# Kernel tuning notes

Measured on AMD Instinct MI355X. Metric: run time of the kernel, lower is better.

## Reference

```python
import jax, jax.numpy as jnp
import numpy as np

WEIGHT = 1.0
BIN_SIZE = 1.0
MAX_MZ = 2000.0
NUM_BINS = int(MAX_MZ / BIN_SIZE)  # 2000
B, N = 8192, 256


def setup_inputs() -> dict:
    key = jax.random.key(0)
    k1, k2, k3, k4, k5 = jax.random.split(key, 5)
    return {
        "pred_mz": jax.random.uniform(k1, (B, N), dtype=jnp.float32),
        "pred_intensity": jax.random.uniform(k2, (B, N), dtype=jnp.float32),
        "target_mz": jax.random.uniform(k3, (B, N), dtype=jnp.float32),
        "target_intensity": jax.random.uniform(k4, (B, N), dtype=jnp.float32),
        "target_mask": jax.random.uniform(k5, (B, N), dtype=jnp.float32),
    }


def _bin_spectrum(mz, intensity):
    # mz is normalized to [0,1]; denormalize and bin. Batched scatter-add:
    # a single 2D indexed add replaces the per-sample scatter_add_ loop.
    bin_idx = jnp.clip((mz * MAX_MZ / BIN_SIZE).astype(jnp.int32), 0, NUM_BINS - 1)  # [B, N]
    bsz = mz.shape[0]
    binned = jnp.zeros((bsz, NUM_BINS), dtype=intensity.dtype)
    return binned.at[jnp.arange(bsz)[:, None], bin_idx].add(intensity)


def reference(pred_mz, pred_intensity, target_mz, target_intensity, target_mask):
    pred_binned = _bin_spectrum(pred_mz, pred_intensity)                    # [B, NUM_BINS]
    target_binned = _bin_spectrum(target_mz, target_intensity * target_mask)
    eps = 1e-8  # matches torch F.cosine_similarity default
    pn = jnp.maximum(jnp.linalg.norm(pred_binned, axis=1), eps)
    tn = jnp.maximum(jnp.linalg.norm(target_binned, axis=1), eps)
    cos = jnp.sum(pred_binned * target_binned, axis=1) / (pn * tn)
    cos = jnp.clip(cos, -1.0, 1.0)
    angle = jnp.arccos(cos)
    loss = jnp.mean(angle / jnp.pi)
    return WEIGHT * loss
```

## Files before the change

kernel.cpp:

```cpp
#include <hip/hip_runtime.h>
#include <math.h>


#define SAL_NUM_BINS 2000
#define SAL_B 8192
#define SAL_N 256
#define SAL_RPB 2
#define SAL_BLOCKS (SAL_B / SAL_RPB)

__global__ __launch_bounds__(256) void sal_row_kernel(
    const float* __restrict__ pred_mz,
    const float* __restrict__ pred_int,
    const float* __restrict__ targ_mz,
    const float* __restrict__ targ_int,
    const float* __restrict__ targ_mask,
    float* __restrict__ row_angle)
{
    __shared__ __align__(16) float hist[SAL_RPB][2][SAL_NUM_BINS];
    __shared__ float rbuf[SAL_RPB][2][3];
    const int t = threadIdx.x;

    {
        float4* h4 = (float4*)&hist[0][0][0];
        const float4 z = make_float4(0.f, 0.f, 0.f, 0.f);
        #pragma unroll
        for (int i = 0; i < 8; ++i) {
            int idx = t + i * 256;
            if (idx < (SAL_RPB * 2 * SAL_NUM_BINS) / 4) h4[idx] = z;
        }
    }
    __syncthreads();

    const int r   = t >> 7;
    const int u   = t & 127;
    const int row = blockIdx.x * SAL_RPB + r;
    const int base = row * SAL_N;

    const float2 pmz = ((const float2*)(pred_mz  + base))[u];
    const float2 pin = ((const float2*)(pred_int + base))[u];
    const float2 tmz = ((const float2*)(targ_mz  + base))[u];
    const float2 tin = ((const float2*)(targ_int + base))[u];
    const float2 tms = ((const float2*)(targ_mask+ base))[u];

    int pb0 = min(max((int)(pmz.x * 2000.0f), 0), SAL_NUM_BINS - 1);
    int pb1 = min(max((int)(pmz.y * 2000.0f), 0), SAL_NUM_BINS - 1);
    int tb0 = min(max((int)(tmz.x * 2000.0f), 0), SAL_NUM_BINS - 1);
    int tb1 = min(max((int)(tmz.y * 2000.0f), 0), SAL_NUM_BINS - 1);
    atomicAdd(&hist[r][0][pb0], pin.x);
    atomicAdd(&hist[r][0][pb1], pin.y);
    atomicAdd(&hist[r][1][tb0], tin.x * tms.x);
    atomicAdd(&hist[r][1][tb1], tin.y * tms.y);
    __syncthreads();

    const float4* p4 = (const float4*)&hist[r][0][0];
    const float4* q4 = (const float4*)&hist[r][1][0];
    float dot = 0.f, p2 = 0.f, t2 = 0.f;
    for (int i = u; i < SAL_NUM_BINS / 4; i += 128) {
        float4 p = p4[i], q = q4[i];
        dot = fmaf(p.x, q.x, dot); p2 = fmaf(p.x, p.x, p2); t2 = fmaf(q.x, q.x, t2);
        dot = fmaf(p.y, q.y, dot); p2 = fmaf(p.y, p.y, p2); t2 = fmaf(q.y, q.y, t2);
        dot = fmaf(p.z, q.z, dot); p2 = fmaf(p.z, p.z, p2); t2 = fmaf(q.z, q.z, t2);
        dot = fmaf(p.w, q.w, dot); p2 = fmaf(p.w, p.w, p2); t2 = fmaf(q.w, q.w, t2);
    }

    for (int off = 32; off > 0; off >>= 1) {
        dot += __shfl_down(dot, off, 64);
        p2  += __shfl_down(p2,  off, 64);
        t2  += __shfl_down(t2,  off, 64);
    }
    const int wir = (t >> 6) & 1;
    if ((t & 63) == 0) {
        rbuf[r][wir][0] = dot; rbuf[r][wir][1] = p2; rbuf[r][wir][2] = t2;
    }
    __syncthreads();
    if (u == 0) {
        float d = rbuf[r][0][0] + rbuf[r][1][0];
        float a = rbuf[r][0][1] + rbuf[r][1][1];
        float c = rbuf[r][0][2] + rbuf[r][1][2];
        float pn = fmaxf(sqrtf(a), 1e-8f);
        float tn = fmaxf(sqrtf(c), 1e-8f);
        float cs = d / (pn * tn);
        cs = fminf(fmaxf(cs, -1.0f), 1.0f);
        row_angle[row] = acosf(cs) * (float)(1.0 / M_PI);
    }
}

__global__ __launch_bounds__(256) void sal_reduce_kernel(
    const float* __restrict__ row_angle, float* __restrict__ out)
{
    const int t = threadIdx.x;
    const float4* ra4 = (const float4*)row_angle;
    float s = 0.0f;
    for (int i = t; i < SAL_B / 4; i += 256) {
        float4 v = ra4[i];
        s += (v.x + v.y) + (v.z + v.w);
    }
    for (int off = 32; off > 0; off >>= 1) s += __shfl_down(s, off, 64);
    __shared__ float rbuf[4];
    const int wave = t >> 6;
    if ((t & 63) == 0) rbuf[wave] = s;
    __syncthreads();
    if (t == 0) out[0] = ((rbuf[0] + rbuf[1]) + (rbuf[2] + rbuf[3])) * (float)(1.0 / SAL_B);
}

extern "C" void kernel_launch(void* const* d_in, const int* in_sizes, int n_in,
                              void* d_out, int out_size, void* d_ws, size_t ws_size,
                              hipStream_t stream) {
    const float* pred_mz   = (const float*)d_in[0];
    const float* pred_int  = (const float*)d_in[1];
    const float* targ_mz   = (const float*)d_in[2];
    const float* targ_int  = (const float*)d_in[3];
    const float* targ_mask = (const float*)d_in[4];
    float* row_angle = (float*)d_ws;
    float* out = (float*)d_out;

    sal_row_kernel<<<SAL_BLOCKS, 256, 0, stream>>>(pred_mz, pred_int, targ_mz,
                                                   targ_int, targ_mask, row_angle);
    sal_reduce_kernel<<<1, 256, 0, stream>>>(row_angle, out);
}
```

Before: 112.5 us.

## Compute cosine terms sparsely from touched bins and process rows sequentially per block

Each block now handles four rows one after another, reusing a single shared-memory histogram pair. After the atomic scatter, each thread gathers the bin values at its own pred and target indices. It computes dot, |p|^2 and |t|^2 as sums of intensity times gathered bin value, which removes the full 2000-bin scan. Only the touched bins are reset before the next row. Per-block angle sums replace per-row outputs, so the final reduce reads fewer values. The trade-off is more __syncthreads per block, since every row is reduced in sequence, and fewer blocks in the grid.

```diff
diff --git a/kernel.cpp b/kernel.cpp
--- a/kernel.cpp
+++ b/kernel.cpp
@@ -5,7 +5,7 @@
 #define SAL_NUM_BINS 2000
 #define SAL_B 8192
 #define SAL_N 256
-#define SAL_RPB 2
+#define SAL_RPB 4
 #define SAL_BLOCKS (SAL_B / SAL_RPB)
 
 __global__ __launch_bounds__(256) void sal_row_kernel(
@@ -14,91 +14,101 @@
     const float* __restrict__ targ_mz,
     const float* __restrict__ targ_int,
     const float* __restrict__ targ_mask,
-    float* __restrict__ row_angle)
+    float* __restrict__ block_partial)
 {
-    __shared__ __align__(16) float hist[SAL_RPB][2][SAL_NUM_BINS];
-    __shared__ float rbuf[SAL_RPB][2][3];
+    __shared__ __align__(16) float hist[2][SAL_NUM_BINS];
+    __shared__ float rbuf[2][4][3];
     const int t = threadIdx.x;
 
     {
-        float4* h4 = (float4*)&hist[0][0][0];
+        float4* h4 = (float4*)&hist[0][0];
         const float4 z = make_float4(0.f, 0.f, 0.f, 0.f);
         #pragma unroll
-        for (int i = 0; i < 8; ++i) {
+        for (int i = 0; i < 4; ++i) {
             int idx = t + i * 256;
-            if (idx < (SAL_RPB * 2 * SAL_NUM_BINS) / 4) h4[idx] = z;
+            if (idx < (2 * SAL_NUM_BINS) / 4) h4[idx] = z;
         }
+    }
+
+    float pmz[SAL_RPB], pin[SAL_RPB], tmz[SAL_RPB], tin[SAL_RPB];
+    #pragma unroll
+    for (int r = 0; r < SAL_RPB; ++r) {
+        const int base = (blockIdx.x * SAL_RPB + r) * SAL_N + t;
+        pmz[r] = pred_mz[base];
+        pin[r] = pred_int[base];
+        tmz[r] = targ_mz[base];
+        tin[r] = targ_int[base] * targ_mask[base];
     }
     __syncthreads();
 
-    const int r   = t >> 7;
-    const int u   = t & 127;
-    const int row = blockIdx.x * SAL_RPB + r;
-    const int base = row * SAL_N;
+    float block_sum = 0.0f;
+    const int wave = t >> 6;
 
-    const float2 pmz = ((const float2*)(pred_mz  + base))[u];
-    const float2 pin = ((const float2*)(pred_int + base))[u];
-    const float2 tmz = ((const float2*)(targ_mz  + base))[u];
-    const float2 tin = ((const float2*)(targ_int + base))[u];
-    const float2 tms = ((const float2*)(targ_mask+ base))[u];
+    #pragma unroll
+    for (int r = 0; r < SAL_RPB; ++r) {
+        const int pb = min(max((int)(pmz[r] * 2000.0f), 0), SAL_NUM_BINS - 1);
+        const int tb = min(max((int)(tmz[r] * 2000.0f), 0), SAL_NUM_BINS - 1);
 
-    int pb0 = min(max((int)(pmz.x * 2000.0f), 0), SAL_NUM_BINS - 1);
-    int pb1 = min(max((int)(pmz.y * 2000.0f), 0), SAL_NUM_BINS - 1);
-    int tb0 = min(max((int)(tmz.x * 2000.0f), 0), SAL_NUM_BINS - 1);
-    int tb1 = min(max((int)(tmz.y * 2000.0f), 0), SAL_NUM_BINS - 1);
-    atomicAdd(&hist[r][0][pb0], pin.x);
-    atomicAdd(&hist[r][0][pb1], pin.y);
-    atomicAdd(&hist[r][1][tb0], tin.x * tms.x);
-    atomicAdd(&hist[r][1][tb1], tin.y * tms.y);
-    __syncthreads();
+        atomicAdd(&hist[0][pb], pin[r]);
+        atomicAdd(&hist[1][tb], tin[r]);
+        __syncthreads();
 
-    const float4* p4 = (const float4*)&hist[r][0][0];
-    const float4* q4 = (const float4*)&hist[r][1][0];
-    float dot = 0.f, p2 = 0.f, t2 = 0.f;
-    for (int i = u; i < SAL_NUM_BINS / 4; i += 128) {
-        float4 p = p4[i], q = q4[i];
-        dot = fmaf(p.x, q.x, dot); p2 = fmaf(p.x, p.x, p2); t2 = fmaf(q.x, q.x, t2);
-        dot = fmaf(p.y, q.y, dot); p2 = fmaf(p.y, p.y, p2); t2 = fmaf(q.y, q.y, t2);
-        dot = fmaf(p.z, q.z, dot); p2 = fmaf(p.z, p.z, p2); t2 = fmaf(q.z, q.z, t2);
-        dot = fmaf(p.w, q.w, dot); p2 = fmaf(p.w, p.w, p2); t2 = fmaf(q.w, q.w, t2);
+        const float pv = hist[0][pb];
+        const float qv = hist[1][pb];
+        const float tv = hist[1][tb];
+        float dot = pin[r] * qv;
+        float p2  = pin[r] * pv;
+        float t2  = tin[r] * tv;
+        __syncthreads();
+
+        hist[0][pb] = 0.0f;
+        hist[1][tb] = 0.0f;
+
+        #pragma unroll
+        for (int off = 32; off > 0; off >>= 1) {
+            dot += __shfl_down(dot, off, 64);
+            p2  += __shfl_down(p2,  off, 64);
+            t2  += __shfl_down(t2,  off, 64);
+        }
+        if ((t & 63) == 0) {
+            rbuf[r & 1][wave][0] = dot;
+            rbuf[r & 1][wave][1] = p2;
+            rbuf[r & 1][wave][2] = t2;
+        }
+        __syncthreads();
+
+        if (t == 0) {
+            float d = (rbuf[r & 1][0][0] + rbuf[r & 1][1][0]) +
+                      (rbuf[r & 1][2][0] + rbuf[r & 1][3][0]);
+            float a = (rbuf[r & 1][0][1] + rbuf[r & 1][1][1]) +
+                      (rbuf[r & 1][2][1] + rbuf[r & 1][3][1]);
+            float c = (rbuf[r & 1][0][2] + rbuf[r & 1][1][2]) +
+                      (rbuf[r & 1][2][2] + rbuf[r & 1][3][2]);
+            float pn = fmaxf(sqrtf(a), 1e-8f);
+            float tn = fmaxf(sqrtf(c), 1e-8f);
+            float cs = d / (pn * tn);
+            cs = fminf(fmaxf(cs, -1.0f), 1.0f);
+            block_sum += acosf(cs) * (float)(1.0 / M_PI);
+        }
     }
-
-    for (int off = 32; off > 0; off >>= 1) {
-        dot += __shfl_down(dot, off, 64);
-        p2  += __shfl_down(p2,  off, 64);
-        t2  += __shfl_down(t2,  off, 64);
-    }
-    const int wir = (t >> 6) & 1;
-    if ((t & 63) == 0) {
-        rbuf[r][wir][0] = dot; rbuf[r][wir][1] = p2; rbuf[r][wir][2] = t2;
-    }
-    __syncthreads();
-    if (u == 0) {
-        float d = rbuf[r][0][0] + rbuf[r][1][0];
-        float a = rbuf[r][0][1] + rbuf[r][1][1];
-        float c = rbuf[r][0][2] + rbuf[r][1][2];
-        float pn = fmaxf(sqrtf(a), 1e-8f);
-        float tn = fmaxf(sqrtf(c), 1e-8f);
-        float cs = d / (pn * tn);
-        cs = fminf(fmaxf(cs, -1.0f), 1.0f);
-        row_angle[row] = acosf(cs) * (float)(1.0 / M_PI);
-    }
+    if (t == 0) block_partial[blockIdx.x] = block_sum;
 }
 
 __global__ __launch_bounds__(256) void sal_reduce_kernel(
-    const float* __restrict__ row_angle, float* __restrict__ out)
+    const float* __restrict__ block_partial, float* __restrict__ out)
 {
     const int t = threadIdx.x;
-    const float4* ra4 = (const float4*)row_angle;
+    const float4* bp4 = (const float4*)block_partial;
     float s = 0.0f;
-    for (int i = t; i < SAL_B / 4; i += 256) {
-        float4 v = ra4[i];
+    #pragma unroll
+    for (int i = 0; i < SAL_BLOCKS / 4 / 256; ++i) {
+        float4 v = bp4[t + i * 256];
         s += (v.x + v.y) + (v.z + v.w);
     }
+    #pragma unroll
     for (int off = 32; off > 0; off >>= 1) s += __shfl_down(s, off, 64);
     __shared__ float rbuf[4];
-    const int wave = t >> 6;
-    if ((t & 63) == 0) rbuf[wave] = s;
+    if ((t & 63) == 0) rbuf[t >> 6] = s;
     __syncthreads();
     if (t == 0) out[0] = ((rbuf[0] + rbuf[1]) + (rbuf[2] + rbuf[3])) * (float)(1.0 / SAL_B);
 }
@@ -111,10 +121,10 @@
     const float* targ_mz   = (const float*)d_in[2];
     const float* targ_int  = (const float*)d_in[3];
     const float* targ_mask = (const float*)d_in[4];
-    float* row_angle = (float*)d_ws;
+    float* block_partial = (float*)d_ws;
     float* out = (float*)d_out;
 
     sal_row_kernel<<<SAL_BLOCKS, 256, 0, stream>>>(pred_mz, pred_int, targ_mz,
-                                                   targ_int, targ_mask, row_angle);
-    sal_reduce_kernel<<<1, 256, 0, stream>>>(row_angle, out);
+                                                   targ_int, targ_mask, block_partial);
+    sal_reduce_kernel<<<1, 256, 0, stream>>>(block_partial, out);
 }
```

Result: no change. 111.4 us (-0.9%).
